# Optimization experiments

Hardware: AMD Instinct MI355X
Metric: run time of the kernel (lower is better)

## Reference

```python
import jax, jax.numpy as jnp
import numpy as np

B_SZ, L, H, P = 16, 1024, 256, 256
DT_MIN, DT_MAX = 1e-3, 1e-1


def setup_inputs() -> dict:
    key = jax.random.key(0)
    ks = jax.random.split(key, 6)
    u = jax.random.normal(ks[0], (B_SZ, L, H), dtype=jnp.float32)
    # Stable diagonal init (stands in for HiPPO-LegS diag: negative real part,
    # spread imaginary parts) so exp(Lambda*Delta) has |.|<1 over long scans.
    Lambda_re = -0.5 * jnp.ones((P,), jnp.float32)
    Lambda_im = jnp.pi * jnp.arange(P, dtype=jnp.float32)
    Bp = jax.random.normal(ks[1], (P, H, 2), jnp.float32) / jnp.sqrt(2.0 * H)  # (P,H,2) real/imag
    Cp = jax.random.normal(ks[2], (H, P, 2), jnp.float32) / jnp.sqrt(2.0 * P)  # (H,P,2) real/imag
    D = jax.random.normal(ks[3], (H,), jnp.float32)
    log_step = (jax.random.uniform(ks[4], (P, 1), jnp.float32)
                * (jnp.log(DT_MAX) - jnp.log(DT_MIN)) + jnp.log(DT_MIN))
    return {"u": u, "Lambda_re": Lambda_re, "Lambda_im": Lambda_im,
            "B": Bp, "C": Cp, "D": D, "log_step": log_step}


def _binop(ei, ej):
    # S5 associative scan element: (A, Bu); compose linear recurrences.
    ai, bi = ei
    aj, bj = ej
    return aj * ai, aj * bi + bj


def reference(u, Lambda_re, Lambda_im, B, C, D, log_step):
    # clip_eigs=False, step_rescale=1.0, conj_sym=True, discretization='zoh'
    Lambda = Lambda_re + 1j * Lambda_im                     # (P,) complex
    B_tilde = B[..., 0] + 1j * B[..., 1]                    # (P,H) complex
    C_tilde = C[..., 0] + 1j * C[..., 1]                    # (H,P) complex
    Delta = jnp.exp(log_step[:, 0])                         # (P,)
    # ZOH discretization
    Lambda_bar = jnp.exp(Lambda * Delta)                    # (P,)
    B_bar = ((Lambda_bar - 1.0) / Lambda)[:, None] * B_tilde  # (P,H)
    # Input projection: (B, L, P) complex
    Bu = jnp.einsum('ph,blh->blp', B_bar, u.astype(B_bar.dtype))
    Lam = jnp.broadcast_to(Lambda_bar, Bu.shape)            # (B, L, P)
    # Parallel associative scan over time axis
    _, xs = jax.lax.associative_scan(_binop, (Lam, Bu), axis=1)  # states (B,L,P)
    # Output projection; conj_sym -> 2 * real part
    ys = 2.0 * jnp.einsum('hp,blp->blh', C_tilde, xs).real  # (B,L,H)
    return ys + D * u                                       # feedthrough
```

## Files before the change

### kernel.cpp

```cpp
#include <hip/hip_runtime.h>
#include <hip/hip_bf16.h>
#include <math.h>

#define BB     16
#define LSEQ   1024
#define HH     256
#define PP     256
#define MROWS  (BB*LSEQ)
#define LC     32
#define NC     (LSEQ/LC)
#define NCHUNK (BB*NC)

#define OFF_W1T  0u
#define OFF_W2T  262144u
#define OFF_PW   524288u
#define OFF_CEND 655360u
#define OFF_CARR 1703936u
#define OFF_XS   2752512u

typedef __attribute__((ext_vector_type(8))) short short8;
typedef __attribute__((ext_vector_type(4))) float floatx4;

__device__ __forceinline__ float bf2f(unsigned hs) {
    union { unsigned u; float f; } v; v.u = hs << 16; return v.f;
}
__device__ __forceinline__ unsigned short f2bs(float f) {
    __hip_bfloat16 h = __float2bfloat16(f);
    union { __hip_bfloat16 h; unsigned short s; } v; v.h = h; return v.s;
}
__device__ __forceinline__ unsigned packbf(float r, float i) {
    return (unsigned)f2bs(r) | ((unsigned)f2bs(i) << 16);
}
__device__ __forceinline__ void async16(const void* g, void* l) {
    __builtin_amdgcn_global_load_lds(
        (const __attribute__((address_space(1))) unsigned*)g,
        (__attribute__((address_space(3))) unsigned*)l, 16, 0, 0);
}
__device__ __forceinline__ float2 lam_pow(float lr, float li, float dtt) {
    float m = expf(lr * dtt);
    return make_float2(m * cosf(li * dtt), m * sinf(li * dtt));
}

__global__ void k_prep(const float* __restrict__ Bm, const float* __restrict__ Cm,
                       const float* __restrict__ Lr, const float* __restrict__ Li,
                       const float* __restrict__ ls, char* __restrict__ ws) {
    int blk = blockIdx.x, t = threadIdx.x;
    if (blk < 256) {
        int p = blk, h = t;
        float lr = Lr[p], li = Li[p];
        float dt = expf(ls[p]);
        float2 lam = lam_pow(lr, li, dt);
        float den = lr * lr + li * li;
        float nr = lam.x - 1.0f, ni = lam.y;
        float cr = (nr * lr + ni * li) / den;
        float ci = (ni * lr - nr * li) / den;
        float br = Bm[(p * HH + h) * 2 + 0];
        float bi = Bm[(p * HH + h) * 2 + 1];
        unsigned short* w1 = (unsigned short*)(ws + OFF_W1T);
        w1[(2 * p) * 256 + h]     = f2bs(cr * br - ci * bi);
        w1[(2 * p + 1) * 256 + h] = f2bs(cr * bi + ci * br);
        if (t <= 32)
            ((float2*)(ws + OFF_PW))[t * 256 + p] = lam_pow(lr, li, dt * (float)t);
    } else {
        int h = blk - 256, p = t;
        float c_r = Cm[(h * PP + p) * 2 + 0];
        float c_i = Cm[(h * PP + p) * 2 + 1];
        ((unsigned*)(ws + OFF_W2T))[h * 256 + p] = packbf(2.0f * c_r, -2.0f * c_i);
    }
}

#define XSTRD 514
#define XSTRS 1028
__global__ __launch_bounds__(512, 4) void k_g1scan(
        const float* __restrict__ u, const float* __restrict__ Lr,
        const float* __restrict__ Li, const float* __restrict__ ls,
        char* __restrict__ ws) {
    extern __shared__ char smem[];
    char* Asb = smem;
    char* Bsb = smem + 4096;
    unsigned short* X = (unsigned short*)smem;
    unsigned* X32 = (unsigned*)smem;
    const unsigned short* W1 = (const unsigned short*)(ws + OFF_W1T);
    const int tid = threadIdx.x, bc = blockIdx.x;
    const int m0 = bc * LC;
    const int wave = tid >> 6, lane = tid & 63;
    const int q = lane >> 4, rr = lane & 15;
    const int c4 = lane & 3, r4 = lane >> 2;

    floatx4 acc[2][4];
    #pragma unroll
    for (int i = 0; i < 2; ++i)
        #pragma unroll
        for (int j = 0; j < 4; ++j) acc[i][j] = (floatx4)0.0f;

    const int arow = tid >> 4, acol4 = (tid & 15) * 4;
    for (int k0 = 0; k0 < 256; k0 += 64) {
        __syncthreads();
        {
            float4 v = *(const float4*)(u + (size_t)(m0 + arow) * 256 + k0 + acol4);
            *(uint2*)(Asb + (acol4 >> 5) * 2048 + arow * 64 + (acol4 & 31) * 2) =
                make_uint2(packbf(v.x, v.y), packbf(v.z, v.w));
        }
        #pragma unroll
        for (int t = 0; t < 8; ++t) {
            int idx = t * 8 + wave;
            int pan = idx & 1, rowg = idx >> 1;
            int row = rowg * 16 + r4;
            async16(W1 + (size_t)row * 256 + k0 + pan * 32 + c4 * 8,
                    Bsb + pan * 32768 + row * 64 + c4 * 16);
        }
        __syncthreads();
        #pragma unroll
        for (int ks = 0; ks < 2; ++ks) {
            short8 a0 = *(const short8*)(Asb + ks * 2048 + rr * 64 + q * 16);
            short8 a1 = *(const short8*)(Asb + ks * 2048 + (16 + rr) * 64 + q * 16);
            #pragma unroll
            for (int j = 0; j < 4; ++j) {
                short8 b = *(const short8*)(Bsb + ks * 32768 +
                                            (wave * 64 + j * 16 + rr) * 64 + q * 16);
                acc[0][j] = __builtin_amdgcn_mfma_f32_16x16x32_bf16(a0, b, acc[0][j], 0, 0, 0);
                acc[1][j] = __builtin_amdgcn_mfma_f32_16x16x32_bf16(a1, b, acc[1][j], 0, 0, 0);
            }
        }
    }
    __syncthreads();
    #pragma unroll
    for (int i = 0; i < 2; ++i)
        #pragma unroll
        for (int j = 0; j < 4; ++j)
            #pragma unroll
            for (int r0 = 0; r0 < 4; ++r0)
                X[(i * 16 + q * 4 + r0) * XSTRS + wave * 64 + j * 16 + rr] =
                    f2bs(acc[i][j][r0]);
    __syncthreads();

    if (tid < 256) {
        const int pq = tid;
        const float2 lam = lam_pow(Lr[pq], Li[pq], expf(ls[pq]));
        unsigned* xs32 = (unsigned*)(ws + OFF_XS);
        float xr = 0.0f, xi = 0.0f;
        #pragma unroll
        for (int j = 0; j < LC; ++j) {
            unsigned cv = X32[j * XSTRD + pq];
            float br = bf2f(cv & 0xffffu), bi = bf2f(cv >> 16);
            float nr = fmaf(lam.x, xr, fmaf(-lam.y, xi, br));
            float ni = fmaf(lam.x, xi, fmaf(lam.y, xr, bi));
            xr = nr; xi = ni;
            xs32[(size_t)(m0 + j) * 256 + pq] = packbf(xr, xi);
        }
        ((float2*)(ws + OFF_CEND))[(size_t)bc * 256 + pq] = make_float2(xr, xi);
    }
}

__global__ void k_carry(const float* __restrict__ Lr, const float* __restrict__ Li,
                        const float* __restrict__ ls, char* __restrict__ ws) {
    const int b = blockIdx.x, p = threadIdx.x;
    const float2* cend = (const float2*)(ws + OFF_CEND);
    float2* carr = (float2*)(ws + OFF_CARR);
    const float2 g = lam_pow(Lr[p], Li[p], expf(ls[p]) * (float)LC);
    float sr = 0.0f, si = 0.0f;
    #pragma unroll
    for (int c = 0; c < NC; ++c) {
        size_t idx = (size_t)(b * NC + c) * 256 + p;
        carr[idx] = make_float2(sr, si);
        float2 e = cend[idx];
        float nr = fmaf(g.x, sr, fmaf(-g.y, si, e.x));
        float ni = fmaf(g.x, si, fmaf(g.y, sr, e.y));
        sr = nr; si = ni;
    }
}

__global__ __launch_bounds__(256, 4) void k_gemm2fix(
        const char* __restrict__ ws_c, const float* __restrict__ D,
        const float* __restrict__ u, float* __restrict__ out) {
    __shared__ char Asb[4096];
    __shared__ char Bsb[32768];
    __shared__ float2 carrs[256];
    const unsigned short* W2 = (const unsigned short*)(ws_c + OFF_W2T);
    const unsigned* xs32 = (const unsigned*)(ws_c + OFF_XS);
    const float2* pw = (const float2*)(ws_c + OFF_PW);
    const float2* carr = (const float2*)(ws_c + OFF_CARR);

    const int tid = threadIdx.x;
    const int wave = tid >> 6, lane = tid & 63;
    const int q = lane >> 4, rr = lane & 15;
    const int c4 = lane & 3, r4 = lane >> 2;
    const int m0 = blockIdx.x * LC;

    carrs[tid] = carr[(size_t)blockIdx.x * 256 + tid];

    floatx4 acc[2][4];
    #pragma unroll
    for (int i = 0; i < 2; ++i)
        #pragma unroll
        for (int j = 0; j < 4; ++j) acc[i][j] = (floatx4)0.0f;

    const int row = tid >> 3, qd = tid & 7;
    const int grow = m0 + row;
    const int jj = (grow & (LC - 1)) + 1;

    for (int k0 = 0; k0 < 512; k0 += 64) {
        __syncthreads();
        {
            int p0 = (k0 >> 1) + qd * 4;
            uint4 xa = *(const uint4*)(xs32 + (size_t)grow * 256 + p0);
            unsigned xv[4] = {xa.x, xa.y, xa.z, xa.w};
            const float2* pwp = pw + (size_t)jj * 256 + p0;
            unsigned o[4];
            #pragma unroll
            for (int e = 0; e < 4; ++e) {
                float2 pwv = pwp[e];
                float2 cav = carrs[p0 + e];
                float fr = pwv.x * cav.x - pwv.y * cav.y;
                float fi = pwv.x * cav.y + pwv.y * cav.x;
                o[e] = packbf(bf2f(xv[e] & 0xffffu) + fr, bf2f(xv[e] >> 16) + fi);
            }
            char* dst = Asb + (qd >> 2) * 2048 + row * 64 + (qd & 3) * 16;
            *(uint4*)dst = make_uint4(o[0], o[1], o[2], o[3]);
        }
        #pragma unroll
        for (int t = 0; t < 8; ++t) {
            int idx = t * 4 + wave;
            int pan = idx & 1, rowg = idx >> 1;
            int rw = rowg * 16 + r4;
            async16(W2 + (size_t)rw * 512 + k0 + pan * 32 + c4 * 8,
                    Bsb + pan * 16384 + rw * 64 + c4 * 16);
        }
        __syncthreads();
        #pragma unroll
        for (int ks = 0; ks < 2; ++ks) {
            short8 a[2], bfr[4];
            #pragma unroll
            for (int i = 0; i < 2; ++i)
                a[i] = *(const short8*)(Asb + ks * 2048 + (i * 16 + rr) * 64 + q * 16);
            #pragma unroll
            for (int j = 0; j < 4; ++j)
                bfr[j] = *(const short8*)(Bsb + ks * 16384 +
                                          (wave * 64 + j * 16 + rr) * 64 + q * 16);
            #pragma unroll
            for (int i = 0; i < 2; ++i)
                #pragma unroll
                for (int j = 0; j < 4; ++j)
                    acc[i][j] = __builtin_amdgcn_mfma_f32_16x16x32_bf16(a[i], bfr[j], acc[i][j], 0, 0, 0);
        }
    }

    #pragma unroll
    for (int i = 0; i < 2; ++i) {
        int mbase = m0 + i * 16 + q * 4;
        #pragma unroll
        for (int j = 0; j < 4; ++j) {
            int col = wave * 64 + j * 16 + rr;
            #pragma unroll
            for (int r0 = 0; r0 < 4; ++r0) {
                int rw = mbase + r0;
                size_t gi = (size_t)rw * 256 + col;
                out[gi] = acc[i][j][r0] + D[col] * u[gi];
            }
        }
    }
}

extern "C" void kernel_launch(void* const* d_in, const int* in_sizes, int n_in,
                              void* d_out, int out_size, void* d_ws, size_t ws_size,
                              hipStream_t stream) {
    const float* u  = (const float*)d_in[0];
    const float* Lr = (const float*)d_in[1];
    const float* Li = (const float*)d_in[2];
    const float* Bm = (const float*)d_in[3];
    const float* Cm = (const float*)d_in[4];
    const float* D  = (const float*)d_in[5];
    const float* ls = (const float*)d_in[6];
    float* out = (float*)d_out;
    char* ws = (char*)d_ws;

    k_prep<<<512, 256, 0, stream>>>(Bm, Cm, Lr, Li, ls, ws);
    k_g1scan<<<NCHUNK, 512, 69632, stream>>>(u, Lr, Li, ls, ws);
    k_carry<<<BB, 256, 0, stream>>>(Lr, Li, ls, ws);
    k_gemm2fix<<<NCHUNK, 256, 0, stream>>>(ws, D, u, out);
}
```

Measured before the change: 113.3 us.

## Fuse all four stages into one persistent kernel with grid barriers

Merges prep, GEMM1+chunk scan, carry propagation and GEMM2 into a single kernel of 512 blocks separated by atomic-counter grid barriers. Chunk-local scan states now stay in shared memory instead of round-tripping through a global xs buffer. The carry fix-up is applied in place in LDS, and the first W2 tile is prefetched before the barrier. Gains come from removing launch gaps and the xs global traffic. In exchange it depends on all 512 blocks being co-resident, which the launch bounds of 4 blocks per CU suggest, and it idles most blocks during the serial carry stage.

```diff
diff --git a/kernel.cpp b/kernel.cpp
--- a/kernel.cpp
+++ b/kernel.cpp
@@ -6,7 +6,6 @@
 #define LSEQ   1024
 #define HH     256
 #define PP     256
-#define MROWS  (BB*LSEQ)
 #define LC     32
 #define NC     (LSEQ/LC)
 #define NCHUNK (BB*NC)
@@ -16,7 +15,7 @@
 #define OFF_PW   524288u
 #define OFF_CEND 655360u
 #define OFF_CARR 1703936u
-#define OFF_XS   2752512u
+#define OFF_BAR  2752512u
 
 typedef __attribute__((ext_vector_type(8))) short short8;
 typedef __attribute__((ext_vector_type(4))) float floatx4;
@@ -41,103 +40,126 @@
     return make_float2(m * cosf(li * dtt), m * sinf(li * dtt));
 }
 
-__global__ void k_prep(const float* __restrict__ Bm, const float* __restrict__ Cm,
-                       const float* __restrict__ Lr, const float* __restrict__ Li,
-                       const float* __restrict__ ls, char* __restrict__ ws) {
-    int blk = blockIdx.x, t = threadIdx.x;
-    if (blk < 256) {
-        int p = blk, h = t;
-        float lr = Lr[p], li = Li[p];
-        float dt = expf(ls[p]);
-        float2 lam = lam_pow(lr, li, dt);
-        float den = lr * lr + li * li;
-        float nr = lam.x - 1.0f, ni = lam.y;
-        float cr = (nr * lr + ni * li) / den;
-        float ci = (ni * lr - nr * li) / den;
-        float br = Bm[(p * HH + h) * 2 + 0];
-        float bi = Bm[(p * HH + h) * 2 + 1];
-        unsigned short* w1 = (unsigned short*)(ws + OFF_W1T);
-        w1[(2 * p) * 256 + h]     = f2bs(cr * br - ci * bi);
-        w1[(2 * p + 1) * 256 + h] = f2bs(cr * bi + ci * br);
-        if (t <= 32)
-            ((float2*)(ws + OFF_PW))[t * 256 + p] = lam_pow(lr, li, dt * (float)t);
-    } else {
-        int h = blk - 256, p = t;
-        float c_r = Cm[(h * PP + p) * 2 + 0];
-        float c_i = Cm[(h * PP + p) * 2 + 1];
-        ((unsigned*)(ws + OFF_W2T))[h * 256 + p] = packbf(2.0f * c_r, -2.0f * c_i);
-    }
-}
-
-#define XSTRD 514
-#define XSTRS 1028
-__global__ __launch_bounds__(512, 4) void k_g1scan(
+__device__ __forceinline__ void gridbar(unsigned* cnt, unsigned target) {
+    __syncthreads();
+    __builtin_amdgcn_fence(__ATOMIC_RELEASE, "agent");
+    if (threadIdx.x == 0) {
+        __hip_atomic_fetch_add(cnt, 1u, __ATOMIC_RELAXED, __HIP_MEMORY_SCOPE_AGENT);
+        for (int it = 0; it < (1 << 20); ++it) {
+            if (__hip_atomic_load(cnt, __ATOMIC_RELAXED, __HIP_MEMORY_SCOPE_AGENT) >= target)
+                break;
+            __builtin_amdgcn_s_sleep(2);
+        }
+    }
+    __syncthreads();
+    __builtin_amdgcn_fence(__ATOMIC_ACQUIRE, "agent");
+}
+
+#define XSTRS 520
+#define XSTRD 260
+#define BSB2_OFF 34816
+#define CARR_OFF 67584
+
+__global__ __launch_bounds__(512, 4) void k_all(
         const float* __restrict__ u, const float* __restrict__ Lr,
         const float* __restrict__ Li, const float* __restrict__ ls,
+        const float* __restrict__ Bm, const float* __restrict__ Cm,
+        const float* __restrict__ D, float* __restrict__ out,
         char* __restrict__ ws) {
     extern __shared__ char smem[];
-    char* Asb = smem;
-    char* Bsb = smem + 4096;
-    unsigned short* X = (unsigned short*)smem;
-    unsigned* X32 = (unsigned*)smem;
-    const unsigned short* W1 = (const unsigned short*)(ws + OFF_W1T);
+    unsigned* bar = (unsigned*)(ws + OFF_BAR);
+
     const int tid = threadIdx.x, bc = blockIdx.x;
-    const int m0 = bc * LC;
     const int wave = tid >> 6, lane = tid & 63;
     const int q = lane >> 4, rr = lane & 15;
     const int c4 = lane & 3, r4 = lane >> 2;
-
-    floatx4 acc[2][4];
-    #pragma unroll
-    for (int i = 0; i < 2; ++i)
-        #pragma unroll
-        for (int j = 0; j < 4; ++j) acc[i][j] = (floatx4)0.0f;
-
-    const int arow = tid >> 4, acol4 = (tid & 15) * 4;
-    for (int k0 = 0; k0 < 256; k0 += 64) {
+    const int m0 = bc * LC;
+
+    if (bc < 256) {
+        if (tid < 256) {
+            int p = bc, h = tid;
+            float lr = Lr[p], li = Li[p];
+            float dt = expf(ls[p]);
+            float2 lam = lam_pow(lr, li, dt);
+            float den = lr * lr + li * li;
+            float nr = lam.x - 1.0f, ni = lam.y;
+            float cr = (nr * lr + ni * li) / den;
+            float ci = (ni * lr - nr * li) / den;
+            float br = Bm[(p * HH + h) * 2 + 0];
+            float bi = Bm[(p * HH + h) * 2 + 1];
+            unsigned short* w1 = (unsigned short*)(ws + OFF_W1T);
+            w1[(2 * p) * 256 + h]     = f2bs(cr * br - ci * bi);
+            w1[(2 * p + 1) * 256 + h] = f2bs(cr * bi + ci * br);
+            if (tid <= 32)
+                ((float2*)(ws + OFF_PW))[tid * 256 + p] = lam_pow(lr, li, dt * (float)tid);
+        }
+    } else {
+        if (tid < 256) {
+            int h = bc - 256, p = tid;
+            float c_r = Cm[(h * PP + p) * 2 + 0];
+            float c_i = Cm[(h * PP + p) * 2 + 1];
+            ((unsigned*)(ws + OFF_W2T))[h * 256 + p] = packbf(2.0f * c_r, -2.0f * c_i);
+        }
+    }
+    gridbar(bar, NCHUNK);
+
+    {
+        char* Asb = smem;
+        char* Bsb = smem + 4096;
+        const unsigned short* W1 = (const unsigned short*)(ws + OFF_W1T);
+        floatx4 acc[2][4];
+        #pragma unroll
+        for (int i = 0; i < 2; ++i)
+            #pragma unroll
+            for (int j = 0; j < 4; ++j) acc[i][j] = (floatx4)0.0f;
+
+        const int arow = tid >> 4, acol4 = (tid & 15) * 4;
+        for (int k0 = 0; k0 < 256; k0 += 64) {
+            __syncthreads();
+            {
+                float4 v = *(const float4*)(u + (size_t)(m0 + arow) * 256 + k0 + acol4);
+                *(uint2*)(Asb + (acol4 >> 5) * 2048 + arow * 64 + (acol4 & 31) * 2) =
+                    make_uint2(packbf(v.x, v.y), packbf(v.z, v.w));
+            }
+            #pragma unroll
+            for (int t = 0; t < 8; ++t) {
+                int idx = t * 8 + wave;
+                int pan = idx & 1, rowg = idx >> 1;
+                int row = rowg * 16 + r4;
+                async16(W1 + (size_t)row * 256 + k0 + pan * 32 + c4 * 8,
+                        Bsb + pan * 32768 + row * 64 + c4 * 16);
+            }
+            __syncthreads();
+            #pragma unroll
+            for (int ks = 0; ks < 2; ++ks) {
+                short8 a0 = *(const short8*)(Asb + ks * 2048 + rr * 64 + q * 16);
+                short8 a1 = *(const short8*)(Asb + ks * 2048 + (16 + rr) * 64 + q * 16);
+                #pragma unroll
+                for (int j = 0; j < 4; ++j) {
+                    short8 b = *(const short8*)(Bsb + ks * 32768 +
+                                                (wave * 64 + j * 16 + rr) * 64 + q * 16);
+                    acc[0][j] = __builtin_amdgcn_mfma_f32_16x16x32_bf16(a0, b, acc[0][j], 0, 0, 0);
+                    acc[1][j] = __builtin_amdgcn_mfma_f32_16x16x32_bf16(a1, b, acc[1][j], 0, 0, 0);
+                }
+            }
+        }
         __syncthreads();
-        {
-            float4 v = *(const float4*)(u + (size_t)(m0 + arow) * 256 + k0 + acol4);
-            *(uint2*)(Asb + (acol4 >> 5) * 2048 + arow * 64 + (acol4 & 31) * 2) =
-                make_uint2(packbf(v.x, v.y), packbf(v.z, v.w));
-        }
-        #pragma unroll
-        for (int t = 0; t < 8; ++t) {
-            int idx = t * 8 + wave;
-            int pan = idx & 1, rowg = idx >> 1;
-            int row = rowg * 16 + r4;
-            async16(W1 + (size_t)row * 256 + k0 + pan * 32 + c4 * 8,
-                    Bsb + pan * 32768 + row * 64 + c4 * 16);
-        }
+        unsigned short* X = (unsigned short*)smem;
+        #pragma unroll
+        for (int i = 0; i < 2; ++i)
+            #pragma unroll
+            for (int j = 0; j < 4; ++j)
+                #pragma unroll
+                for (int r0 = 0; r0 < 4; ++r0)
+                    X[(i * 16 + q * 4 + r0) * XSTRS + wave * 64 + j * 16 + rr] =
+                        f2bs(acc[i][j][r0]);
         __syncthreads();
-        #pragma unroll
-        for (int ks = 0; ks < 2; ++ks) {
-            short8 a0 = *(const short8*)(Asb + ks * 2048 + rr * 64 + q * 16);
-            short8 a1 = *(const short8*)(Asb + ks * 2048 + (16 + rr) * 64 + q * 16);
-            #pragma unroll
-            for (int j = 0; j < 4; ++j) {
-                short8 b = *(const short8*)(Bsb + ks * 32768 +
-                                            (wave * 64 + j * 16 + rr) * 64 + q * 16);
-                acc[0][j] = __builtin_amdgcn_mfma_f32_16x16x32_bf16(a0, b, acc[0][j], 0, 0, 0);
-                acc[1][j] = __builtin_amdgcn_mfma_f32_16x16x32_bf16(a1, b, acc[1][j], 0, 0, 0);
-            }
-        }
-    }
-    __syncthreads();
-    #pragma unroll
-    for (int i = 0; i < 2; ++i)
-        #pragma unroll
-        for (int j = 0; j < 4; ++j)
-            #pragma unroll
-            for (int r0 = 0; r0 < 4; ++r0)
-                X[(i * 16 + q * 4 + r0) * XSTRS + wave * 64 + j * 16 + rr] =
-                    f2bs(acc[i][j][r0]);
-    __syncthreads();
+    }
 
     if (tid < 256) {
         const int pq = tid;
         const float2 lam = lam_pow(Lr[pq], Li[pq], expf(ls[pq]));
-        unsigned* xs32 = (unsigned*)(ws + OFF_XS);
+        unsigned* X32 = (unsigned*)smem;
         float xr = 0.0f, xi = 0.0f;
         #pragma unroll
         for (int j = 0; j < LC; ++j) {
@@ -146,116 +168,118 @@
             float nr = fmaf(lam.x, xr, fmaf(-lam.y, xi, br));
             float ni = fmaf(lam.x, xi, fmaf(lam.y, xr, bi));
             xr = nr; xi = ni;
-            xs32[(size_t)(m0 + j) * 256 + pq] = packbf(xr, xi);
+            X32[j * XSTRD + pq] = packbf(xr, xi);
         }
         ((float2*)(ws + OFF_CEND))[(size_t)bc * 256 + pq] = make_float2(xr, xi);
-    }
-}
-
-__global__ void k_carry(const float* __restrict__ Lr, const float* __restrict__ Li,
-                        const float* __restrict__ ls, char* __restrict__ ws) {
-    const int b = blockIdx.x, p = threadIdx.x;
-    const float2* cend = (const float2*)(ws + OFF_CEND);
-    float2* carr = (float2*)(ws + OFF_CARR);
-    const float2 g = lam_pow(Lr[p], Li[p], expf(ls[p]) * (float)LC);
-    float sr = 0.0f, si = 0.0f;
-    #pragma unroll
-    for (int c = 0; c < NC; ++c) {
-        size_t idx = (size_t)(b * NC + c) * 256 + p;
-        carr[idx] = make_float2(sr, si);
-        float2 e = cend[idx];
-        float nr = fmaf(g.x, sr, fmaf(-g.y, si, e.x));
-        float ni = fmaf(g.x, si, fmaf(g.y, sr, e.y));
-        sr = nr; si = ni;
-    }
-}
-
-__global__ __launch_bounds__(256, 4) void k_gemm2fix(
-        const char* __restrict__ ws_c, const float* __restrict__ D,
-        const float* __restrict__ u, float* __restrict__ out) {
-    __shared__ char Asb[4096];
-    __shared__ char Bsb[32768];
-    __shared__ float2 carrs[256];
-    const unsigned short* W2 = (const unsigned short*)(ws_c + OFF_W2T);
-    const unsigned* xs32 = (const unsigned*)(ws_c + OFF_XS);
-    const float2* pw = (const float2*)(ws_c + OFF_PW);
-    const float2* carr = (const float2*)(ws_c + OFF_CARR);
-
-    const int tid = threadIdx.x;
-    const int wave = tid >> 6, lane = tid & 63;
-    const int q = lane >> 4, rr = lane & 15;
-    const int c4 = lane & 3, r4 = lane >> 2;
-    const int m0 = blockIdx.x * LC;
-
-    carrs[tid] = carr[(size_t)blockIdx.x * 256 + tid];
-
-    floatx4 acc[2][4];
-    #pragma unroll
-    for (int i = 0; i < 2; ++i)
-        #pragma unroll
-        for (int j = 0; j < 4; ++j) acc[i][j] = (floatx4)0.0f;
-
-    const int row = tid >> 3, qd = tid & 7;
-    const int grow = m0 + row;
-    const int jj = (grow & (LC - 1)) + 1;
-
-    for (int k0 = 0; k0 < 512; k0 += 64) {
+    } else {
+        const unsigned short* W2 = (const unsigned short*)(ws + OFF_W2T);
+        char* Bsb2 = smem + BSB2_OFF;
+        int w4 = wave - 4;
+        #pragma unroll
+        for (int t = 0; t < 8; ++t) {
+            int idx = t * 4 + w4;
+            int pan = idx & 1, rowg = idx >> 1;
+            int row = rowg * 16 + r4;
+            async16(W2 + (size_t)row * 512 + pan * 32 + c4 * 8,
+                    Bsb2 + pan * 16384 + row * 64 + c4 * 16);
+        }
+    }
+    gridbar(bar, 2 * NCHUNK);
+
+    if (bc < BB && tid < 256) {
+        const int b = bc, p = tid;
+        const float2* cend = (const float2*)(ws + OFF_CEND);
+        float2* carr = (float2*)(ws + OFF_CARR);
+        const float2 g = lam_pow(Lr[p], Li[p], expf(ls[p]) * (float)LC);
+        float sr = 0.0f, si = 0.0f;
+        #pragma unroll
+        for (int c = 0; c < NC; ++c) {
+            size_t idx = (size_t)(b * NC + c) * 256 + p;
+            carr[idx] = make_float2(sr, si);
+            float2 e = cend[idx];
+            float nr = fmaf(g.x, sr, fmaf(-g.y, si, e.x));
+            float ni = fmaf(g.x, si, fmaf(g.y, sr, e.y));
+            sr = nr; si = ni;
+        }
+    }
+    gridbar(bar, 3 * NCHUNK);
+
+    {
+        float2* carrs = (float2*)(smem + CARR_OFF);
+        if (tid < 256)
+            carrs[tid] = ((const float2*)(ws + OFF_CARR))[(size_t)bc * 256 + tid];
         __syncthreads();
-        {
-            int p0 = (k0 >> 1) + qd * 4;
-            uint4 xa = *(const uint4*)(xs32 + (size_t)grow * 256 + p0);
-            unsigned xv[4] = {xa.x, xa.y, xa.z, xa.w};
-            const float2* pwp = pw + (size_t)jj * 256 + p0;
-            unsigned o[4];
-            #pragma unroll
-            for (int e = 0; e < 4; ++e) {
-                float2 pwv = pwp[e];
-                float2 cav = carrs[p0 + e];
-                float fr = pwv.x * cav.x - pwv.y * cav.y;
-                float fi = pwv.x * cav.y + pwv.y * cav.x;
-                o[e] = packbf(bf2f(xv[e] & 0xffffu) + fr, bf2f(xv[e] >> 16) + fi);
-            }
-            char* dst = Asb + (qd >> 2) * 2048 + row * 64 + (qd & 3) * 16;
-            *(uint4*)dst = make_uint4(o[0], o[1], o[2], o[3]);
-        }
-        #pragma unroll
-        for (int t = 0; t < 8; ++t) {
-            int idx = t * 4 + wave;
-            int pan = idx & 1, rowg = idx >> 1;
-            int rw = rowg * 16 + r4;
-            async16(W2 + (size_t)rw * 512 + k0 + pan * 32 + c4 * 8,
-                    Bsb + pan * 16384 + rw * 64 + c4 * 16);
-        }
-        __syncthreads();
-        #pragma unroll
-        for (int ks = 0; ks < 2; ++ks) {
-            short8 a[2], bfr[4];
-            #pragma unroll
-            for (int i = 0; i < 2; ++i)
-                a[i] = *(const short8*)(Asb + ks * 2048 + (i * 16 + rr) * 64 + q * 16);
-            #pragma unroll
-            for (int j = 0; j < 4; ++j)
-                bfr[j] = *(const short8*)(Bsb + ks * 16384 +
-                                          (wave * 64 + j * 16 + rr) * 64 + q * 16);
-            #pragma unroll
-            for (int i = 0; i < 2; ++i)
-                #pragma unroll
-                for (int j = 0; j < 4; ++j)
-                    acc[i][j] = __builtin_amdgcn_mfma_f32_16x16x32_bf16(a[i], bfr[j], acc[i][j], 0, 0, 0);
-        }
-    }
-
-    #pragma unroll
-    for (int i = 0; i < 2; ++i) {
-        int mbase = m0 + i * 16 + q * 4;
-        #pragma unroll
-        for (int j = 0; j < 4; ++j) {
-            int col = wave * 64 + j * 16 + rr;
-            #pragma unroll
-            for (int r0 = 0; r0 < 4; ++r0) {
-                int rw = mbase + r0;
-                size_t gi = (size_t)rw * 256 + col;
-                out[gi] = acc[i][j][r0] + D[col] * u[gi];
+        unsigned* X32 = (unsigned*)smem;
+        const float2* pw = (const float2*)(ws + OFF_PW);
+        const int frow = tid >> 4, fcol = tid & 15;
+        const float2* pwr = pw + (size_t)(frow + 1) * 256;
+        #pragma unroll 4
+        for (int e = 0; e < 16; ++e) {
+            int p = fcol + e * 16;
+            unsigned cv = X32[frow * XSTRD + p];
+            float2 pwv = pwr[p];
+            float2 cav = carrs[p];
+            float fr = pwv.x * cav.x - pwv.y * cav.y;
+            float fi = pwv.x * cav.y + pwv.y * cav.x;
+            X32[frow * XSTRD + p] =
+                packbf(bf2f(cv & 0xffffu) + fr, bf2f(cv >> 16) + fi);
+        }
+    }
+
+    {
+        const unsigned short* W2 = (const unsigned short*)(ws + OFF_W2T);
+        char* Bsb2 = smem + BSB2_OFF;
+        const char* Xb = (const char*)smem;
+        floatx4 acc[2][2];
+        #pragma unroll
+        for (int i = 0; i < 2; ++i)
+            #pragma unroll
+            for (int j = 0; j < 2; ++j) acc[i][j] = (floatx4)0.0f;
+
+        for (int k0 = 0; k0 < 512; k0 += 64) {
+            if (k0) {
+                __syncthreads();
+                #pragma unroll
+                for (int t = 0; t < 4; ++t) {
+                    int idx = t * 8 + wave;
+                    int pan = idx & 1, rowg = idx >> 1;
+                    int row = rowg * 16 + r4;
+                    async16(W2 + (size_t)row * 512 + k0 + pan * 32 + c4 * 8,
+                            Bsb2 + pan * 16384 + row * 64 + c4 * 16);
+                }
+            }
+            __syncthreads();
+            #pragma unroll
+            for (int ks = 0; ks < 2; ++ks) {
+                short8 a[2], bfr[2];
+                #pragma unroll
+                for (int i = 0; i < 2; ++i)
+                    a[i] = *(const short8*)(Xb + (i * 16 + rr) * (XSTRS * 2) +
+                                            k0 * 2 + ks * 64 + q * 16);
+                #pragma unroll
+                for (int j = 0; j < 2; ++j)
+                    bfr[j] = *(const short8*)(Bsb2 + ks * 16384 +
+                                              (wave * 32 + j * 16 + rr) * 64 + q * 16);
+                #pragma unroll
+                for (int i = 0; i < 2; ++i)
+                    #pragma unroll
+                    for (int j = 0; j < 2; ++j)
+                        acc[i][j] = __builtin_amdgcn_mfma_f32_16x16x32_bf16(a[i], bfr[j], acc[i][j], 0, 0, 0);
+            }
+        }
+
+        #pragma unroll
+        for (int i = 0; i < 2; ++i) {
+            int mbase = m0 + i * 16 + q * 4;
+            #pragma unroll
+            for (int j = 0; j < 2; ++j) {
+                int col = wave * 32 + j * 16 + rr;
+                #pragma unroll
+                for (int r0 = 0; r0 < 4; ++r0) {
+                    int rw = mbase + r0;
+                    size_t gi = (size_t)rw * 256 + col;
+                    out[gi] = acc[i][j][r0] + D[col] * u[gi];
+                }
             }
         }
     }
@@ -274,8 +298,6 @@
     float* out = (float*)d_out;
     char* ws = (char*)d_ws;
 
-    k_prep<<<512, 256, 0, stream>>>(Bm, Cm, Lr, Li, ls, ws);
-    k_g1scan<<<NCHUNK, 512, 69632, stream>>>(u, Lr, Li, ls, ws);
-    k_carry<<<BB, 256, 0, stream>>>(Lr, Li, ls, ws);
-    k_gemm2fix<<<NCHUNK, 256, 0, stream>>>(ws, D, u, out);
-}
+    hipMemsetAsync(ws + OFF_BAR, 0, 64, stream);
+    k_all<<<NCHUNK, 512, 69632, stream>>>(u, Lr, Li, ls, Bm, Cm, D, out, ws);
+}
```

Measured after the change: 369.6 us. 3.26x slower.
